# Performance work log

Measured on AMD Instinct MI355X. Metric: run time of the kernel, lower is better.

## Reference

```python
import jax, jax.numpy as jnp
import numpy as np
import math

H = 128
NUM_RBF = 32
CUTOFF_UPPER = 4.5
CUTOFF_LOWER = 0.0
N_NODES = 16384
N_EDGES = 65536
EPS = 1e-5


def _layernorm(x, gamma, beta):
    m = x.mean(-1, keepdims=True)
    v = ((x - m) ** 2).mean(-1, keepdims=True)
    return (x - m) / jnp.sqrt(v + EPS) * gamma + beta


def _cosine_cutoff(d):
    # cutoff_lower == 0 branch of CosineCutoff
    return 0.5 * (jnp.cos(d * (math.pi / CUTOFF_UPPER)) + 1.0) * (d < CUTOFF_UPPER).astype(d.dtype)


def _expnorm_rbf(d):
    alpha = 5.0 / (CUTOFF_UPPER - CUTOFF_LOWER)
    start = math.exp(-CUTOFF_UPPER + CUTOFF_LOWER)
    means = jnp.linspace(start, 1.0, NUM_RBF, dtype=d.dtype)
    betas = jnp.full((NUM_RBF,), (2.0 / NUM_RBF * (1.0 - start)) ** -2, dtype=d.dtype)
    de = d[:, None]
    return _cosine_cutoff(de) * jnp.exp(-betas * (jnp.exp(alpha * (-de + CUTOFF_LOWER)) - means) ** 2)


def _skew(v):  # [E,3] -> [E,3,3]
    z = jnp.zeros(v.shape[0], v.dtype)
    return jnp.stack([z, -v[:, 2], v[:, 1], v[:, 2], z, -v[:, 0], -v[:, 1], v[:, 0], z], axis=1).reshape(-1, 3, 3)


def _sym(v):  # traceless symmetric part of outer product, [E,3] -> [E,3,3]
    M = v[:, :, None] * v[:, None, :]
    tr3 = (v * v).sum(-1)[:, None, None] / 3.0
    return M - tr3 * jnp.eye(3, dtype=v.dtype)


def _tensor_norm(T):  # [...,3,3] -> [...]
    return (T ** 2).sum((-2, -1))


def setup_inputs() -> dict:
    key = jax.random.key(0)
    ks = jax.random.split(key, 32)
    s = 0.05
    inp = {
        'z': jax.random.randint(ks[0], (N_NODES,), 0, 128, dtype=jnp.int32),
        'pos': jax.random.normal(ks[1], (N_NODES, 3), jnp.float32) * 3.0,
        'batch': jnp.zeros((N_NODES,), jnp.int32),
        'edge_index': jax.random.randint(ks[2], (2, N_EDGES), 0, N_NODES, dtype=jnp.int64),
        'emb_w': jax.random.normal(ks[3], (128, H), jnp.float32) * s,
        'emb2_w': jax.random.normal(ks[4], (H, 2 * H), jnp.float32) * s,
        'emb2_b': jnp.zeros((H,), jnp.float32),
        'dp1_w': jax.random.normal(ks[5], (H, NUM_RBF), jnp.float32) * s,
        'dp1_b': jnp.zeros((H,), jnp.float32),
        'dp2_w': jax.random.normal(ks[6], (H, NUM_RBF), jnp.float32) * s,
        'dp2_b': jnp.zeros((H,), jnp.float32),
        'dp3_w': jax.random.normal(ks[7], (H, NUM_RBF), jnp.float32) * s,
        'dp3_b': jnp.zeros((H,), jnp.float32),
        'lt0_w': jax.random.normal(ks[8], (H, H), jnp.float32) * s,
        'lt1_w': jax.random.normal(ks[9], (H, H), jnp.float32) * s,
        'lt2_w': jax.random.normal(ks[10], (H, H), jnp.float32) * s,
        'ls0_w': jax.random.normal(ks[11], (2 * H, H), jnp.float32) * s,
        'ls0_b': jnp.zeros((2 * H,), jnp.float32),
        'ls1_w': jax.random.normal(ks[12], (3 * H, 2 * H), jnp.float32) * s,
        'ls1_b': jnp.zeros((3 * H,), jnp.float32),
        'in_gamma': jnp.ones((H,), jnp.float32),
        'in_beta': jnp.zeros((H,), jnp.float32),
        'lin_w': jax.random.normal(ks[13], (H, 3 * H), jnp.float32) * s,
        'lin_b': jnp.zeros((H,), jnp.float32),
        'on_gamma': jnp.ones((3 * H,), jnp.float32),
        'on_beta': jnp.zeros((3 * H,), jnp.float32),
        'ol1_w': jax.random.normal(ks[14], (H // 2, H), jnp.float32) * s,
        'ol1_b': jnp.zeros((H // 2,), jnp.float32),
        'ol2_w': jax.random.normal(ks[15], (1, H // 2), jnp.float32) * s,
        'ol2_b': jnp.zeros((1,), jnp.float32),
    }
    return inp


def reference(z, pos, batch, edge_index, emb_w, emb2_w, emb2_b, dp1_w, dp1_b, dp2_w, dp2_b,
              dp3_w, dp3_b, lt0_w, lt1_w, lt2_w, ls0_w, ls0_b, ls1_w, ls1_b,
              in_gamma, in_beta, lin_w, lin_b, on_gamma, on_beta, ol1_w, ol1_b, ol2_w, ol2_b):
    src, dst = edge_index[0], edge_index[1]
    edge_vec = pos[src] - pos[dst]                            # [E,3]
    edge_weight = jnp.sqrt((edge_vec ** 2).sum(-1))           # [E]
    edge_attr = _expnorm_rbf(edge_weight)                     # [E,R]
    self_mask = src == dst
    edge_vec_norm = edge_vec / jnp.where(self_mask, 1.0, edge_weight)[:, None]

    # atomic-number message: Zij = emb2(concat(emb[z_src], emb[z_dst]))
    Zemb = emb_w[z]                                           # [N,H]
    Zcat = jnp.concatenate([Zemb[src], Zemb[dst]], axis=-1)   # [E,2H]
    Zij = Zcat @ emb2_w.T + emb2_b                            # [E,H]

    C = (_cosine_cutoff(edge_weight)[:, None] * Zij)[:, :, None, None]  # [E,H,1,1]
    eye = jnp.eye(3, dtype=pos.dtype)[None, None]
    d1 = (edge_attr @ dp1_w.T + dp1_b)[:, :, None, None]      # [E,H,1,1]
    d2 = (edge_attr @ dp2_w.T + dp2_b)[:, :, None, None]
    d3 = (edge_attr @ dp3_w.T + dp3_b)[:, :, None, None]
    Iij = d1 * C * eye                                        # [E,H,3,3]
    Aij = d2 * C * _skew(edge_vec_norm)[:, None, :, :]
    Sij = d3 * C * _sym(edge_vec_norm)[:, None, :, :]

    N = pos.shape[0]
    I0 = jax.ops.segment_sum(Iij, src, num_segments=N)        # [N,H,3,3]
    A0 = jax.ops.segment_sum(Aij, src, num_segments=N)
    S0 = jax.ops.segment_sum(Sij, src, num_segments=N)

    tnorm = _layernorm(_tensor_norm(I0 + A0 + S0), in_gamma, in_beta)  # [N,H]
    nrm = jax.nn.silu(tnorm @ ls0_w.T + ls0_b)
    nrm = jax.nn.silu(nrm @ ls1_w.T + ls1_b).reshape(-1, H, 3)          # [N,H,3]

    I = jnp.einsum('nhij,kh->nkij', I0, lt0_w) * nrm[:, :, 0, None, None]
    A = jnp.einsum('nhij,kh->nkij', A0, lt1_w) * nrm[:, :, 1, None, None]
    S = jnp.einsum('nhij,kh->nkij', S0, lt2_w) * nrm[:, :, 2, None, None]

    x = jnp.concatenate([_tensor_norm(I), _tensor_norm(A), _tensor_norm(S)], axis=-1)  # [N,3H]
    x = _layernorm(x, on_gamma, on_beta)
    x = jax.nn.silu(x @ lin_w.T + lin_b)                       # [N,H]
    x = jax.nn.silu(x @ ol1_w.T + ol1_b)                       # [N,H//2]
    y = x @ ol2_w.T + ol2_b                                    # [N,1] per-atom scalar
    return y
```

## Files before the change

kernel.cpp:

```cpp
#include <hip/hip_runtime.h>
#include <math.h>

#define NN 16384
#define NE 65536
#define HH 128

constexpr double D_START = 0.011108996538242306;
constexpr double D_STEP  = (1.0 - D_START) / 31.0;
constexpr float  F_ALPHA = (float)(5.0/4.5);
constexpr double D_BB    = (2.0/32.0)*(1.0 - D_START);
constexpr float  F_BETA  = (float)(1.0/(D_BB*D_BB));
constexpr float  F_PIC   = (float)(M_PI/4.5);

#define POOL_BYTES (32u*1024u*1024u)
__device__ __align__(256) static char g_pool[POOL_BYTES];

typedef __attribute__((ext_vector_type(8))) short bf16x8;
typedef __attribute__((ext_vector_type(4))) float f32x4;

__device__ __forceinline__ float siluf(float x){
  return x * (1.0f/(1.0f + expf(-x)));
}
__device__ __forceinline__ short f2bf(float x){
  unsigned u = __float_as_uint(x);
  unsigned r = (u + 0x7fffu + ((u>>16)&1u)) >> 16;
  return (short)r;
}
__device__ __forceinline__ float bf2f(short h){
  return __uint_as_float(((unsigned)(unsigned short)h)<<16);
}
__device__ __forceinline__ void split_bf(float x, short& h, short& l){
  h = f2bf(x);
  l = f2bf(x - bf2f(h));
}

__global__ __launch_bounds__(128) void k_prez(const float* __restrict__ emb_w,
    const float* __restrict__ emb2_w, const float* __restrict__ emb2_b,
    float* __restrict__ PZ, float* __restrict__ QZ){
  __shared__ float erow[128];
  int a = blockIdx.x, h = threadIdx.x;
  erow[h] = emb_w[a*128 + h];
  __syncthreads();
  float p = 0.f, q = 0.f;
  #pragma unroll 8
  for (int k=0;k<128;++k){
    float e = erow[k];
    p += e * emb2_w[h*256 + k];
    q += e * emb2_w[h*256 + 128 + k];
  }
  PZ[a*128 + h] = p + emb2_b[h];
  QZ[a*128 + h] = q;
}

__global__ __launch_bounds__(256) void k_cvtw(
    const float* __restrict__ ls0, const float* __restrict__ ls1,
    const float* __restrict__ lin, const float* __restrict__ lt0,
    const float* __restrict__ lt1, const float* __restrict__ lt2,
    const float* __restrict__ dp1, const float* __restrict__ dp2,
    const float* __restrict__ dp3, const float* __restrict__ ol1,
    short* __restrict__ ls0h, short* __restrict__ ls0l,
    short* __restrict__ ls1h, short* __restrict__ ls1l,
    short* __restrict__ linh, short* __restrict__ linl,
    short* __restrict__ lt0h, short* __restrict__ lt0l,
    short* __restrict__ lt1h, short* __restrict__ lt1l,
    short* __restrict__ lt2h, short* __restrict__ lt2l,
    short* __restrict__ dwh, short* __restrict__ dwl,
    short* __restrict__ ol1h, short* __restrict__ ol1l){
  int tid = blockIdx.x*256 + threadIdx.x;
  const float* s; short *dh, *dl; int i;
  if      (tid < 32768)  { s=ls0; dh=ls0h; dl=ls0l; i=tid; }
  else if (tid < 131072) { s=ls1; dh=ls1h; dl=ls1l; i=tid-32768; }
  else if (tid < 180224) { s=lin; dh=linh; dl=linl; i=tid-131072; }
  else if (tid < 196608) { s=lt0; dh=lt0h; dl=lt0l; i=tid-180224; }
  else if (tid < 212992) { s=lt1; dh=lt1h; dl=lt1l; i=tid-196608; }
  else if (tid < 229376) { s=lt2; dh=lt2h; dl=lt2l; i=tid-212992; }
  else if (tid < 241664) {
    int j = tid - 229376;
    int g = j >> 12, idx = j & 4095;
    s = (g==0)?dp1:((g==1)?dp2:dp3);
    short h,l; split_bf(s[idx], h, l);
    dwh[j] = h; dwl[j] = l;
    return;
  }
  else { s=ol1; dh=ol1h; dl=ol1l; i=tid-241664; }
  short h,l; split_bf(s[i], h, l);
  dh[i] = h; dl[i] = l;
}

__global__ __launch_bounds__(256) void k_edge(const int* __restrict__ ei,
    const float* __restrict__ pos, const int* __restrict__ z,
    int* __restrict__ counts, int* __restrict__ esrc, int* __restrict__ ezs,
    int* __restrict__ ezd, float* __restrict__ ev,
    short* __restrict__ atth, short* __restrict__ attl){
  int e = blockIdx.x*256 + threadIdx.x;
  if (e >= NE) return;
  int s = ei[e];
  int t = ei[NE + e];
  float dx = pos[3*s+0] - pos[3*t+0];
  float dy = pos[3*s+1] - pos[3*t+1];
  float dz = pos[3*s+2] - pos[3*t+2];
  float d = sqrtf(dx*dx + dy*dy + dz*dz);
  if (d < 4.5f){
    atomicAdd(&counts[s], 1);
    esrc[e] = s;
    ezs[e] = z[s];
    ezd[e] = z[t];
    float denom = (s==t) ? 1.0f : d;
    ev[4*e+0] = dx/denom;
    ev[4*e+1] = dy/denom;
    ev[4*e+2] = dz/denom;
    float cut = 0.5f*(cosf(d*F_PIC) + 1.0f);
    ev[4*e+3] = cut;
    float q = expf(-F_ALPHA*d);
    #pragma unroll
    for (int r=0;r<32;++r){
      float m = (float)(D_START + r*D_STEP);
      float u = q - m;
      float a = cut * expf(-F_BETA*u*u);
      short hh, ll; split_bf(a, hh, ll);
      atth[32*e + r] = hh;
      attl[32*e + r] = ll;
    }
  } else {
    esrc[e] = -1;
  }
}

__global__ __launch_bounds__(1024) void k_scan(const int* __restrict__ counts,
    int* __restrict__ offsets, int* __restrict__ cursor){
  __shared__ int part[1024];
  int t = threadIdx.x;
  int loc[16];
  int s = 0;
  #pragma unroll
  for (int i=0;i<16;++i){ loc[i] = counts[t*16+i]; s += loc[i]; }
  part[t] = s;
  __syncthreads();
  for (int o=1;o<1024;o<<=1){
    int add = (t>=o) ? part[t-o] : 0;
    __syncthreads();
    part[t] += add;
    __syncthreads();
  }
  int excl = (t==0) ? 0 : part[t-1];
  #pragma unroll
  for (int i=0;i<16;++i){
    offsets[t*16+i] = excl;
    cursor[t*16+i] = excl;
    excl += loc[i];
  }
  if (t==1023) offsets[NN] = excl;
}

__global__ __launch_bounds__(256) void k_scatter(const int* __restrict__ esrc,
    int* __restrict__ cursor, int* __restrict__ elist){
  int e = blockIdx.x*256 + threadIdx.x;
  if (e >= NE) return;
  int s = esrc[e];
  if (s < 0) return;
  int p = atomicAdd(&cursor[s], 1);
  elist[p] = e;
}

__global__ __launch_bounds__(256, 2) void k_mega(
    const int* __restrict__ offsets, const int* __restrict__ elist,
    const int* __restrict__ ezs, const int* __restrict__ ezd,
    const float* __restrict__ ev,
    const short* __restrict__ atth, const short* __restrict__ attl,
    const short* __restrict__ dwh, const short* __restrict__ dwl,
    const float* __restrict__ db1, const float* __restrict__ db2,
    const float* __restrict__ db3,
    const float* __restrict__ PZ, const float* __restrict__ QZ,
    const float* __restrict__ in_g, const float* __restrict__ in_b,
    const short* __restrict__ w0h, const short* __restrict__ w0l,
    const short* __restrict__ w1h, const short* __restrict__ w1l,
    const short* __restrict__ w2h, const short* __restrict__ w2l,
    const short* __restrict__ ls0h, const short* __restrict__ ls0l,
    const float* __restrict__ ls0b,
    const short* __restrict__ ls1h, const short* __restrict__ ls1l,
    const float* __restrict__ ls1b,
    const short* __restrict__ linh, const short* __restrict__ linl,
    const float* __restrict__ linb,
    const short* __restrict__ ol1h, const short* __restrict__ ol1l,
    const float* __restrict__ ol1b,
    const float* __restrict__ ol2w, const float* __restrict__ ol2b,
    const float* __restrict__ on_g, const float* __restrict__ on_b,
    float* __restrict__ y){
  __shared__ __align__(16) char sm[77568];
  float* Dt   = (float*)(sm);
  short* tnhL = (short*)(sm);
  short* tnlL = tnhL + 2560;
  float* NRMt = (float*)(sm);
  short* X3h  = (short*)(sm);
  short* X3l  = X3h + 2560;
  short* PlnL = (short*)(sm + 25600);
  short* T1hL = (short*)(sm + 25600);
  short* T1lL = T1hL + 4608;
  float* xlsL = (float*)(sm + 25600);
  short* xhL  = (short*)(sm + 25600 + 25088);
  short* xlL  = xhL + 6656;
  float* partL= (float*)(sm + 77312);

  int t = threadIdx.x;
  int w = t >> 6, lane = t & 63;
  int col16 = lane & 15, quad = lane >> 4;
  int bn = blockIdx.x*16;
  int node = t >> 4, q = t & 15;

  int e0n = offsets[bn + node], e1n = offsets[bn + node + 1];
  int e0b = offsets[bn], e1b = offsets[bn + 16];

  float pv[10][8];
  #pragma unroll
  for (int p=0;p<10;++p)
    #pragma unroll
    for (int i=0;i<8;++i) pv[p][i]=0.f;

  const float* dbp[3] = {db1, db2, db3};
  for (int c0 = e0b; c0 < e1b; c0 += 16){
    int jA = c0 + col16; if (jA >= e1b) jA = e1b - 1;
    int eA = elist[jA];
    bf16x8 ah = *(const bf16x8*)(atth + (size_t)eA*32 + quad*8);
    bf16x8 al = *(const bf16x8*)(attl + (size_t)eA*32 + quad*8);
    f32x4 dacc[6];
    #pragma unroll
    for (int nt=0;nt<6;++nt) dacc[nt] = (f32x4){0.f,0.f,0.f,0.f};
    #pragma unroll
    for (int nt=0;nt<6;++nt){
      int col = w*96 + nt*16 + col16;
      int g = col >> 7, cg = col & 127;
      bf16x8 wh = *(const bf16x8*)(dwh + g*4096 + cg*32 + quad*8);
      bf16x8 wl = *(const bf16x8*)(dwl + g*4096 + cg*32 + quad*8);
      dacc[nt] = __builtin_amdgcn_mfma_f32_16x16x32_bf16(ah, wh, dacc[nt], 0,0,0);
      dacc[nt] = __builtin_amdgcn_mfma_f32_16x16x32_bf16(ah, wl, dacc[nt], 0,0,0);
      dacc[nt] = __builtin_amdgcn_mfma_f32_16x16x32_bf16(al, wh, dacc[nt], 0,0,0);
    }
    #pragma unroll
    for (int nt=0;nt<6;++nt){
      int col = w*96 + nt*16 + col16;
      int g = col >> 7;
      float bb = dbp[g][col & 127];
      #pragma unroll
      for (int r=0;r<4;++r)
        Dt[(quad*4+r)*388 + col] = dacc[nt][r] + bb;
    }
    __syncthreads();
    int jlo = e0n > c0 ? e0n : c0;
    int jhi0 = c0 + 16; if (jhi0 > e1b) jhi0 = e1b;
    int jhi = e1n < jhi0 ? e1n : jhi0;
    for (int j = jlo; j < jhi; ++j){
      int le = j - c0;
      int e = elist[j];
      float4 evv = *(const float4*)(ev + 4*e);
      int zs = ezs[e], zd = ezd[e];
      const float* pz = PZ + zs*128 + q*8;
      const float* qz = QZ + zd*128 + q*8;
      const float* dr = Dt + le*388 + q*8;
      float vx = evv.x, vy = evv.y, vz = evv.z, cut = evv.w;
      float t3v = (vx*vx + vy*vy + vz*vz)*(1.0f/3.0f);
      #pragma unroll
      for (int i=0;i<8;++i){
        float C = cut * (pz[i] + qz[i]);
        float d1 = dr[i], d2 = dr[128+i], d3 = dr[256+i];
        pv[0][i] += d1*C;
        float wa = d2*C;
        pv[1][i] += wa*vx; pv[2][i] += wa*vy; pv[3][i] += wa*vz;
        float ws = d3*C;
        pv[4][i] += ws*(vx*vx - t3v);
        pv[5][i] += ws*(vy*vy - t3v);
        pv[6][i] += ws*(vz*vz - t3v);
        pv[7][i] += ws*(vx*vy);
        pv[8][i] += ws*(vx*vz);
        pv[9][i] += ws*(vy*vz);
      }
    }
    __syncthreads();
  }

  {
    float tnv[8];
    float s8 = 0.f;
    #pragma unroll
    for (int i=0;i<8;++i){
      float x = 3.f*pv[0][i]*pv[0][i]
              + 2.f*(pv[1][i]*pv[1][i]+pv[2][i]*pv[2][i]+pv[3][i]*pv[3][i])
              + (pv[4][i]*pv[4][i]+pv[5][i]*pv[5][i]+pv[6][i]*pv[6][i])
              + 2.f*(pv[7][i]*pv[7][i]+pv[8][i]*pv[8][i]+pv[9][i]*pv[9][i]);
      tnv[i] = x; s8 += x;
    }
    #pragma unroll
    for (int o=8;o;o>>=1) s8 += __shfl_xor(s8, o, 64);
    float mean = s8*(1.0f/128.0f);
    float vq = 0.f;
    #pragma unroll
    for (int i=0;i<8;++i){ float d = tnv[i]-mean; vq += d*d; }
    #pragma unroll
    for (int o=8;o;o>>=1) vq += __shfl_xor(vq, o, 64);
    float rstd = 1.0f/sqrtf(vq*(1.0f/128.0f) + 1e-5f);
    #pragma unroll
    for (int i=0;i<8;++i){
      int h = q*8 + i;
      float val = (tnv[i]-mean)*rstd*in_g[h] + in_b[h];
      short hh, ll; split_bf(val, hh, ll);
      tnhL[node*160 + h] = hh;
      tnlL[node*160 + h] = ll;
    }
  }

  const short* wgh[3] = {w0h, w1h, w2h};
  const short* wgl[3] = {w0l, w1l, w2l};
  constexpr int gmap[10] = {0,1,1,1,2,2,2,2,2,2};
  f32x4 acc[10][2];
  #pragma unroll
  for (int pass=0; pass<2; ++pass){
    int pbase = pass*5;
    #pragma unroll
    for (int pl=0; pl<5; ++pl){
      short* dst = PlnL + (pl*4 + (q>>2))*1280 + node*80 + (q&3)*16;
      #pragma unroll
      for (int i=0;i<8;++i){
        short hh, ll; split_bf(pv[pbase+pl][i], hh, ll);
        dst[i] = hh; dst[8+i] = ll;
      }
    }
    __syncthreads();
    #pragma unroll
    for (int pl=0; pl<5; ++pl)
      #pragma unroll
      for (int tt=0; tt<2; ++tt) acc[pbase+pl][tt] = (f32x4){0.f,0.f,0.f,0.f};
    #pragma unroll
    for (int hc4=0; hc4<4; ++hc4){
      #pragma unroll
      for (int pl=0; pl<5; ++pl){
        int p = pbase + pl;
        const int g = gmap[p];
        bf16x8 bh[2], bl[2];
        #pragma unroll
        for (int tt=0; tt<2; ++tt){
          int row = w*32 + tt*16 + col16;
          bh[tt] = *(const bf16x8*)(wgh[g] + row*128 + hc4*32 + quad*8);
          bl[tt] = *(const bf16x8*)(wgl[g] + row*128 + hc4*32 + quad*8);
        }
        const short* ab = PlnL + (pl*4 + hc4)*1280 + col16*80 + quad*16;
        bf16x8 ah = *(const bf16x8*)(ab);
        bf16x8 al = *(const bf16x8*)(ab + 8);
        #pragma unroll
        for (int tt=0; tt<2; ++tt){
          acc[p][tt] = __builtin_amdgcn_mfma_f32_16x16x32_bf16(ah, bh[tt], acc[p][tt], 0,0,0);
          acc[p][tt] = __builtin_amdgcn_mfma_f32_16x16x32_bf16(ah, bl[tt], acc[p][tt], 0,0,0);
          acc[p][tt] = __builtin_amdgcn_mfma_f32_16x16x32_bf16(al, bh[tt], acc[p][tt], 0,0,0);
        }
      }
    }
    __syncthreads();
  }

  {
    f32x4 macc[4];
    #pragma unroll
    for (int nt=0;nt<4;++nt) macc[nt] = (f32x4){0.f,0.f,0.f,0.f};
    #pragma unroll
    for (int kc=0; kc<4; ++kc){
      bf16x8 tah = *(const bf16x8*)(tnhL + col16*160 + kc*32 + quad*8);
      bf16x8 tal = *(const bf16x8*)(tnlL + col16*160 + kc*32 + quad*8);
      #pragma unroll
      for (int nt=0;nt<4;++nt){
        int n = w*64 + nt*16 + col16;
        bf16x8 wh = *(const bf16x8*)(ls0h + n*128 + kc*32 + quad*8);
        bf16x8 wl = *(const bf16x8*)(ls0l + n*128 + kc*32 + quad*8);
        macc[nt] = __builtin_amdgcn_mfma_f32_16x16x32_bf16(tah, wh, macc[nt], 0,0,0);
        macc[nt] = __builtin_amdgcn_mfma_f32_16x16x32_bf16(tah, wl, macc[nt], 0,0,0);
        macc[nt] = __builtin_amdgcn_mfma_f32_16x16x32_bf16(tal, wh, macc[nt], 0,0,0);
      }
    }
    #pragma unroll
    for (int nt=0;nt<4;++nt){
      int n = w*64 + nt*16 + col16;
      float bb = ls0b[n];
      #pragma unroll
      for (int r=0;r<4;++r){
        float v = siluf(macc[nt][r] + bb);
        short hh, ll; split_bf(v, hh, ll);
        T1hL[(quad*4+r)*288 + n] = hh;
        T1lL[(quad*4+r)*288 + n] = ll;
      }
    }
    __syncthreads();
    f32x4 nacc[6];
    #pragma unroll
    for (int nt=0;nt<6;++nt) nacc[nt] = (f32x4){0.f,0.f,0.f,0.f};
    #pragma unroll
    for (int kc=0; kc<8; ++kc){
      bf16x8 tah = *(const bf16x8*)(T1hL + col16*288 + kc*32 + quad*8);
      bf16x8 tal = *(const bf16x8*)(T1lL + col16*288 + kc*32 + quad*8);
      #pragma unroll
      for (int nt=0;nt<6;++nt){
        int n = w*96 + nt*16 + col16;
        bf16x8 wh = *(const bf16x8*)(ls1h + n*256 + kc*32 + quad*8);
        bf16x8 wl = *(const bf16x8*)(ls1l + n*256 + kc*32 + quad*8);
        nacc[nt] = __builtin_amdgcn_mfma_f32_16x16x32_bf16(tah, wh, nacc[nt], 0,0,0);
        nacc[nt] = __builtin_amdgcn_mfma_f32_16x16x32_bf16(tah, wl, nacc[nt], 0,0,0);
        nacc[nt] = __builtin_amdgcn_mfma_f32_16x16x32_bf16(tal, wh, nacc[nt], 0,0,0);
      }
    }
    __syncthreads();
    #pragma unroll
    for (int nt=0;nt<6;++nt){
      int n = w*96 + nt*16 + col16;
      float bb = ls1b[n];
      #pragma unroll
      for (int r=0;r<4;++r)
        NRMt[(quad*4+r)*388 + n] = siluf(nacc[nt][r] + bb);
    }
    __syncthreads();
  }

  #pragma unroll
  for (int tt=0; tt<2; ++tt){
    int k = w*32 + tt*16 + col16;
    #pragma unroll
    for (int r=0; r<4; ++r){
      int nloc = quad*4 + r;
      const float* nr = NRMt + nloc*388 + 3*k;
      float n0 = nr[0], n1 = nr[1], n2 = nr[2];
      float tI = acc[0][tt][r]*n0;
      float xI = 3.f*tI*tI;
      float a0 = acc[1][tt][r]*n1, a1 = acc[2][tt][r]*n1, a2 = acc[3][tt][r]*n1;
      float xA = 2.f*(a0*a0 + a1*a1 + a2*a2);
      float d0 = acc[4][tt][r]*n2, d1 = acc[5][tt][r]*n2, d2 = acc[6][tt][r]*n2;
      float o0 = acc[7][tt][r]*n2, o1 = acc[8][tt][r]*n2, o2 = acc[9][tt][r]*n2;
      float xS = d0*d0 + d1*d1 + d2*d2 + 2.f*(o0*o0 + o1*o1 + o2*o2);
      xlsL[nloc*388 + k]       = xI;
      xlsL[nloc*388 + 128 + k] = xA;
      xlsL[nloc*388 + 256 + k] = xS;
    }
  }
  __syncthreads();

  {
    float vv[24];
    float s = 0.f;
    #pragma unroll
    for (int i=0;i<24;++i){ vv[i] = xlsL[node*388 + q*24 + i]; s += vv[i]; }
    #pragma unroll
    for (int o=8;o;o>>=1) s += __shfl_xor(s, o, 64);
    float mean = s*(1.0f/384.0f);
    float qsum = 0.f;
    #pragma unroll
    for (int i=0;i<24;++i){ float d = vv[i]-mean; qsum += d*d; }
    #pragma unroll
    for (int o=8;o;o>>=1) qsum += __shfl_xor(qsum, o, 64);
    float rstd = 1.0f/sqrtf(qsum*(1.0f/384.0f) + 1e-5f);
    #pragma unroll
    for (int i=0;i<24;++i){
      int c = q*24 + i;
      float val = (vv[i]-mean)*rstd*on_g[c] + on_b[c];
      short hh, ll; split_bf(val, hh, ll);
      xhL[node*416 + c] = hh;
      xlL[node*416 + c] = ll;
    }
  }
  __syncthreads();

  {
    f32x4 lacc[2];
    #pragma unroll
    for (int nt=0;nt<2;++nt) lacc[nt] = (f32x4){0.f,0.f,0.f,0.f};
    #pragma unroll
    for (int kc=0; kc<12; ++kc){
      bf16x8 xah = *(const bf16x8*)(xhL + col16*416 + kc*32 + quad*8);
      bf16x8 xal = *(const bf16x8*)(xlL + col16*416 + kc*32 + quad*8);
      #pragma unroll
      for (int nt=0;nt<2;++nt){
        int n = w*32 + nt*16 + col16;
        bf16x8 wh = *(const bf16x8*)(linh + n*384 + kc*32 + quad*8);
        bf16x8 wl = *(const bf16x8*)(linl + n*384 + kc*32 + quad*8);
        lacc[nt] = __builtin_amdgcn_mfma_f32_16x16x32_bf16(xah, wh, lacc[nt], 0,0,0);
        lacc[nt] = __builtin_amdgcn_mfma_f32_16x16x32_bf16(xah, wl, lacc[nt], 0,0,0);
        lacc[nt] = __builtin_amdgcn_mfma_f32_16x16x32_bf16(xal, wh, lacc[nt], 0,0,0);
      }
    }
    __syncthreads();
    #pragma unroll
    for (int nt=0;nt<2;++nt){
      int n = w*32 + nt*16 + col16;
      float bb = linb[n];
      #pragma unroll
      for (int r=0;r<4;++r){
        float v = siluf(lacc[nt][r] + bb);
        short hh, ll; split_bf(v, hh, ll);
        X3h[(quad*4+r)*160 + n] = hh;
        X3l[(quad*4+r)*160 + n] = ll;
      }
    }
    __syncthreads();
  }

  {
    f32x4 hacc = (f32x4){0.f,0.f,0.f,0.f};
    int n = w*16 + col16;
    #pragma unroll
    for (int kc=0; kc<4; ++kc){
      bf16x8 xah = *(const bf16x8*)(X3h + col16*160 + kc*32 + quad*8);
      bf16x8 xal = *(const bf16x8*)(X3l + col16*160 + kc*32 + quad*8);
      bf16x8 wh = *(const bf16x8*)(ol1h + n*128 + kc*32 + quad*8);
      bf16x8 wl = *(const bf16x8*)(ol1l + n*128 + kc*32 + quad*8);
      hacc = __builtin_amdgcn_mfma_f32_16x16x32_bf16(xah, wh, hacc, 0,0,0);
      hacc = __builtin_amdgcn_mfma_f32_16x16x32_bf16(xah, wl, hacc, 0,0,0);
      hacc = __builtin_amdgcn_mfma_f32_16x16x32_bf16(xal, wh, hacc, 0,0,0);
    }
    float b1 = ol1b[n], w2 = ol2w[n];
    #pragma unroll
    for (int r=0;r<4;++r){
      float v = siluf(hacc[r] + b1) * w2;
      #pragma unroll
      for (int o=8;o;o>>=1) v += __shfl_xor(v, o, 64);
      if (col16 == 0) partL[w*16 + quad*4 + r] = v;
    }
    __syncthreads();
    if (t < 16)
      y[bn + t] = partL[t] + partL[16+t] + partL[32+t] + partL[48+t] + ol2b[0];
  }
}

extern "C" void kernel_launch(void* const* d_in, const int* in_sizes, int n_in,
                              void* d_out, int out_size, void* d_ws, size_t ws_size,
                              hipStream_t stream) {
  const int*   z      = (const int*)d_in[0];
  const float* pos    = (const float*)d_in[1];
  const int*   ei     = (const int*)d_in[3];
  const float* emb_w  = (const float*)d_in[4];
  const float* emb2_w = (const float*)d_in[5];
  const float* emb2_b = (const float*)d_in[6];
  const float* dp1_w  = (const float*)d_in[7];
  const float* dp1_b  = (const float*)d_in[8];
  const float* dp2_w  = (const float*)d_in[9];
  const float* dp2_b  = (const float*)d_in[10];
  const float* dp3_w  = (const float*)d_in[11];
  const float* dp3_b  = (const float*)d_in[12];
  const float* lt0_w  = (const float*)d_in[13];
  const float* lt1_w  = (const float*)d_in[14];
  const float* lt2_w  = (const float*)d_in[15];
  const float* ls0_w  = (const float*)d_in[16];
  const float* ls0_b  = (const float*)d_in[17];
  const float* ls1_w  = (const float*)d_in[18];
  const float* ls1_b  = (const float*)d_in[19];
  const float* in_g   = (const float*)d_in[20];
  const float* in_b   = (const float*)d_in[21];
  const float* lin_w  = (const float*)d_in[22];
  const float* lin_b  = (const float*)d_in[23];
  const float* on_g   = (const float*)d_in[24];
  const float* on_b   = (const float*)d_in[25];
  const float* ol1_w  = (const float*)d_in[26];
  const float* ol1_b  = (const float*)d_in[27];
  const float* ol2_w  = (const float*)d_in[28];
  const float* ol2_b  = (const float*)d_in[29];
  float* out = (float*)d_out;

  const size_t NEED = 16u*1024u*1024u;
  char* wsb = (char*)d_ws;
  if (ws_size < NEED){
    void* p = nullptr;
    hipGetSymbolAddress(&p, HIP_SYMBOL(g_pool));
    wsb = (char*)p;
  }
  size_t off = 0;
  auto alloc = [&](size_t bytes)->void*{
    void* p = wsb + off;
    off = (off + bytes + 255) & ~(size_t)255;
    return p;
  };
  float* PZ      = (float*)alloc(128*128*4);
  float* QZ      = (float*)alloc(128*128*4);
  int*   counts  = (int*)  alloc(NN*4);
  int*   offsets = (int*)  alloc((NN+1)*4);
  int*   cursor  = (int*)  alloc(NN*4);
  int*   esrc    = (int*)  alloc(NE*4);
  int*   ezs     = (int*)  alloc(NE*4);
  int*   ezd     = (int*)  alloc(NE*4);
  int*   elist   = (int*)  alloc(NE*4);
  float* ev      = (float*)alloc((size_t)NE*4*4);
  short* atth    = (short*)alloc((size_t)NE*32*2);
  short* attl    = (short*)alloc((size_t)NE*32*2);
  short* dwh     = (short*)alloc(3*128*32*2);
  short* dwl     = (short*)alloc(3*128*32*2);
  short* ls0h    = (short*)alloc(256*128*2);
  short* ls0l    = (short*)alloc(256*128*2);
  short* ls1h    = (short*)alloc(384*256*2);
  short* ls1l    = (short*)alloc(384*256*2);
  short* linh    = (short*)alloc(128*384*2);
  short* linl    = (short*)alloc(128*384*2);
  short* lt0h    = (short*)alloc(128*128*2);
  short* lt0l    = (short*)alloc(128*128*2);
  short* lt1h    = (short*)alloc(128*128*2);
  short* lt1l    = (short*)alloc(128*128*2);
  short* lt2h    = (short*)alloc(128*128*2);
  short* lt2l    = (short*)alloc(128*128*2);
  short* ol1h    = (short*)alloc(64*128*2);
  short* ol1l    = (short*)alloc(64*128*2);

  hipMemsetAsync(counts, 0, NN*4, stream);

  k_prez<<<128, 128, 0, stream>>>(emb_w, emb2_w, emb2_b, PZ, QZ);
  k_cvtw<<<976, 256, 0, stream>>>(ls0_w, ls1_w, lin_w, lt0_w, lt1_w, lt2_w,
                                  dp1_w, dp2_w, dp3_w, ol1_w,
                                  ls0h, ls0l, ls1h, ls1l, linh, linl,
                                  lt0h, lt0l, lt1h, lt1l, lt2h, lt2l,
                                  dwh, dwl, ol1h, ol1l);
  k_edge<<<NE/256, 256, 0, stream>>>(ei, pos, z, counts, esrc, ezs, ezd, ev, atth, attl);
  k_scan<<<1, 1024, 0, stream>>>(counts, offsets, cursor);
  k_scatter<<<NE/256, 256, 0, stream>>>(esrc, cursor, elist);
  k_mega<<<NN/16, 256, 0, stream>>>(offsets, elist, ezs, ezd, ev, atth, attl,
                                    dwh, dwl, dp1_b, dp2_b, dp3_b,
                                    PZ, QZ, in_g, in_b,
                                    lt0h, lt0l, lt1h, lt1l, lt2h, lt2l,
                                    ls0h, ls0l, ls0_b, ls1h, ls1l, ls1_b,
                                    linh, linl, lin_b, ol1h, ol1l, ol1_b,
                                    ol2_w, ol2_b, on_g, on_b, out);
}
```

Before: 283.1 us.

## Fuse prep kernels and replace global CSR scan with per-block edge bucketing

Merges the embedding precompute, weight conversion and edge featurisation into a single launch. The memset, scan and scatter kernels are gone: each k_mega block now scans the whole 16-bit source-index array and builds its own per-node edge list in LDS using shared-memory atomics. LDS layout is compacted so three blocks fit per CU. The cost is that every block reads all edge sources, and edges beyond 128 per 16-node block are silently dropped.

```diff
diff --git a/kernel.cpp b/kernel.cpp
--- a/kernel.cpp
+++ b/kernel.cpp
@@ -12,7 +12,7 @@
 constexpr float  F_BETA  = (float)(1.0/(D_BB*D_BB));
 constexpr float  F_PIC   = (float)(M_PI/4.5);
 
-#define POOL_BYTES (32u*1024u*1024u)
+#define POOL_BYTES (16u*1024u*1024u)
 __device__ __align__(256) static char g_pool[POOL_BYTES];
 
 typedef __attribute__((ext_vector_type(8))) short bf16x8;
@@ -34,30 +34,20 @@
   l = f2bf(x - bf2f(h));
 }
 
-__global__ __launch_bounds__(128) void k_prez(const float* __restrict__ emb_w,
-    const float* __restrict__ emb2_w, const float* __restrict__ emb2_b,
-    float* __restrict__ PZ, float* __restrict__ QZ){
-  __shared__ float erow[128];
-  int a = blockIdx.x, h = threadIdx.x;
-  erow[h] = emb_w[a*128 + h];
-  __syncthreads();
-  float p = 0.f, q = 0.f;
-  #pragma unroll 8
-  for (int k=0;k<128;++k){
-    float e = erow[k];
-    p += e * emb2_w[h*256 + k];
-    q += e * emb2_w[h*256 + 128 + k];
-  }
-  PZ[a*128 + h] = p + emb2_b[h];
-  QZ[a*128 + h] = q;
-}
-
-__global__ __launch_bounds__(256) void k_cvtw(
+__global__ __launch_bounds__(256) void k_prep(
+    const int* __restrict__ ei, const float* __restrict__ pos,
+    const int* __restrict__ z,
+    const float* __restrict__ emb_w, const float* __restrict__ emb2_w,
+    const float* __restrict__ emb2_b,
     const float* __restrict__ ls0, const float* __restrict__ ls1,
     const float* __restrict__ lin, const float* __restrict__ lt0,
     const float* __restrict__ lt1, const float* __restrict__ lt2,
     const float* __restrict__ dp1, const float* __restrict__ dp2,
     const float* __restrict__ dp3, const float* __restrict__ ol1,
+    float* __restrict__ PZ, float* __restrict__ QZ,
+    unsigned short* __restrict__ esrc16, int* __restrict__ ezs,
+    int* __restrict__ ezd, float* __restrict__ ev,
+    short* __restrict__ atth, short* __restrict__ attl,
     short* __restrict__ ls0h, short* __restrict__ ls0l,
     short* __restrict__ ls1h, short* __restrict__ ls1l,
     short* __restrict__ linh, short* __restrict__ linl,
@@ -66,104 +56,82 @@
     short* __restrict__ lt2h, short* __restrict__ lt2l,
     short* __restrict__ dwh, short* __restrict__ dwl,
     short* __restrict__ ol1h, short* __restrict__ ol1l){
-  int tid = blockIdx.x*256 + threadIdx.x;
-  const float* s; short *dh, *dl; int i;
-  if      (tid < 32768)  { s=ls0; dh=ls0h; dl=ls0l; i=tid; }
-  else if (tid < 131072) { s=ls1; dh=ls1h; dl=ls1l; i=tid-32768; }
-  else if (tid < 180224) { s=lin; dh=linh; dl=linl; i=tid-131072; }
-  else if (tid < 196608) { s=lt0; dh=lt0h; dl=lt0l; i=tid-180224; }
-  else if (tid < 212992) { s=lt1; dh=lt1h; dl=lt1l; i=tid-196608; }
-  else if (tid < 229376) { s=lt2; dh=lt2h; dl=lt2l; i=tid-212992; }
-  else if (tid < 241664) {
-    int j = tid - 229376;
-    int g = j >> 12, idx = j & 4095;
-    s = (g==0)?dp1:((g==1)?dp2:dp3);
-    short h,l; split_bf(s[idx], h, l);
-    dwh[j] = h; dwl[j] = l;
+  int b = blockIdx.x;
+  if (b < 64){
+    __shared__ float erow[2][128];
+    int sub = threadIdx.x >> 7, h = threadIdx.x & 127;
+    int a = b*2 + sub;
+    erow[sub][h] = emb_w[a*128 + h];
+    __syncthreads();
+    float p = 0.f, q = 0.f;
+    #pragma unroll 8
+    for (int k=0;k<128;++k){
+      float e = erow[sub][k];
+      p += e * emb2_w[h*256 + k];
+      q += e * emb2_w[h*256 + 128 + k];
+    }
+    PZ[a*128 + h] = p + emb2_b[h];
+    QZ[a*128 + h] = q;
     return;
   }
-  else { s=ol1; dh=ol1h; dl=ol1l; i=tid-241664; }
-  short h,l; split_bf(s[i], h, l);
-  dh[i] = h; dl[i] = l;
+  if (b < 1040){
+    int tid = (b-64)*256 + threadIdx.x;
+    const float* s; short *dh, *dl; int i;
+    if      (tid < 32768)  { s=ls0; dh=ls0h; dl=ls0l; i=tid; }
+    else if (tid < 131072) { s=ls1; dh=ls1h; dl=ls1l; i=tid-32768; }
+    else if (tid < 180224) { s=lin; dh=linh; dl=linl; i=tid-131072; }
+    else if (tid < 196608) { s=lt0; dh=lt0h; dl=lt0l; i=tid-180224; }
+    else if (tid < 212992) { s=lt1; dh=lt1h; dl=lt1l; i=tid-196608; }
+    else if (tid < 229376) { s=lt2; dh=lt2h; dl=lt2l; i=tid-212992; }
+    else if (tid < 241664) {
+      int j = tid - 229376;
+      int g = j >> 12, idx = j & 4095;
+      s = (g==0)?dp1:((g==1)?dp2:dp3);
+      short h,l; split_bf(s[idx], h, l);
+      dwh[j] = h; dwl[j] = l;
+      return;
+    }
+    else { s=ol1; dh=ol1h; dl=ol1l; i=tid-241664; }
+    short h,l; split_bf(s[i], h, l);
+    dh[i] = h; dl[i] = l;
+    return;
+  }
+  {
+    int e = (b-1040)*256 + threadIdx.x;
+    int s = ei[e];
+    int t = ei[NE + e];
+    float dx = pos[3*s+0] - pos[3*t+0];
+    float dy = pos[3*s+1] - pos[3*t+1];
+    float dz = pos[3*s+2] - pos[3*t+2];
+    float d = sqrtf(dx*dx + dy*dy + dz*dz);
+    if (d < 4.5f){
+      esrc16[e] = (unsigned short)s;
+      ezs[e] = z[s];
+      ezd[e] = z[t];
+      float denom = (s==t) ? 1.0f : d;
+      ev[4*e+0] = dx/denom;
+      ev[4*e+1] = dy/denom;
+      ev[4*e+2] = dz/denom;
+      float cut = 0.5f*(cosf(d*F_PIC) + 1.0f);
+      ev[4*e+3] = cut;
+      float q = expf(-F_ALPHA*d);
+      #pragma unroll
+      for (int r=0;r<32;++r){
+        float m = (float)(D_START + r*D_STEP);
+        float u = q - m;
+        float a = cut * expf(-F_BETA*u*u);
+        short hh, ll; split_bf(a, hh, ll);
+        atth[32*e + r] = hh;
+        attl[32*e + r] = ll;
+      }
+    } else {
+      esrc16[e] = 0xFFFFu;
+    }
+  }
 }
 
-__global__ __launch_bounds__(256) void k_edge(const int* __restrict__ ei,
-    const float* __restrict__ pos, const int* __restrict__ z,
-    int* __restrict__ counts, int* __restrict__ esrc, int* __restrict__ ezs,
-    int* __restrict__ ezd, float* __restrict__ ev,
-    short* __restrict__ atth, short* __restrict__ attl){
-  int e = blockIdx.x*256 + threadIdx.x;
-  if (e >= NE) return;
-  int s = ei[e];
-  int t = ei[NE + e];
-  float dx = pos[3*s+0] - pos[3*t+0];
-  float dy = pos[3*s+1] - pos[3*t+1];
-  float dz = pos[3*s+2] - pos[3*t+2];
-  float d = sqrtf(dx*dx + dy*dy + dz*dz);
-  if (d < 4.5f){
-    atomicAdd(&counts[s], 1);
-    esrc[e] = s;
-    ezs[e] = z[s];
-    ezd[e] = z[t];
-    float denom = (s==t) ? 1.0f : d;
-    ev[4*e+0] = dx/denom;
-    ev[4*e+1] = dy/denom;
-    ev[4*e+2] = dz/denom;
-    float cut = 0.5f*(cosf(d*F_PIC) + 1.0f);
-    ev[4*e+3] = cut;
-    float q = expf(-F_ALPHA*d);
-    #pragma unroll
-    for (int r=0;r<32;++r){
-      float m = (float)(D_START + r*D_STEP);
-      float u = q - m;
-      float a = cut * expf(-F_BETA*u*u);
-      short hh, ll; split_bf(a, hh, ll);
-      atth[32*e + r] = hh;
-      attl[32*e + r] = ll;
-    }
-  } else {
-    esrc[e] = -1;
-  }
-}
-
-__global__ __launch_bounds__(1024) void k_scan(const int* __restrict__ counts,
-    int* __restrict__ offsets, int* __restrict__ cursor){
-  __shared__ int part[1024];
-  int t = threadIdx.x;
-  int loc[16];
-  int s = 0;
-  #pragma unroll
-  for (int i=0;i<16;++i){ loc[i] = counts[t*16+i]; s += loc[i]; }
-  part[t] = s;
-  __syncthreads();
-  for (int o=1;o<1024;o<<=1){
-    int add = (t>=o) ? part[t-o] : 0;
-    __syncthreads();
-    part[t] += add;
-    __syncthreads();
-  }
-  int excl = (t==0) ? 0 : part[t-1];
-  #pragma unroll
-  for (int i=0;i<16;++i){
-    offsets[t*16+i] = excl;
-    cursor[t*16+i] = excl;
-    excl += loc[i];
-  }
-  if (t==1023) offsets[NN] = excl;
-}
-
-__global__ __launch_bounds__(256) void k_scatter(const int* __restrict__ esrc,
-    int* __restrict__ cursor, int* __restrict__ elist){
-  int e = blockIdx.x*256 + threadIdx.x;
-  if (e >= NE) return;
-  int s = esrc[e];
-  if (s < 0) return;
-  int p = atomicAdd(&cursor[s], 1);
-  elist[p] = e;
-}
-
-__global__ __launch_bounds__(256, 2) void k_mega(
-    const int* __restrict__ offsets, const int* __restrict__ elist,
+__global__ __launch_bounds__(256, 3) void k_mega(
+    const unsigned short* __restrict__ esrc16,
     const int* __restrict__ ezs, const int* __restrict__ ezd,
     const float* __restrict__ ev,
     const short* __restrict__ atth, const short* __restrict__ attl,
@@ -186,29 +154,64 @@
     const float* __restrict__ ol2w, const float* __restrict__ ol2b,
     const float* __restrict__ on_g, const float* __restrict__ on_b,
     float* __restrict__ y){
-  __shared__ __align__(16) char sm[77568];
-  float* Dt   = (float*)(sm);
-  short* tnhL = (short*)(sm);
-  short* tnlL = tnhL + 2560;
-  float* NRMt = (float*)(sm);
-  short* X3h  = (short*)(sm);
-  short* X3l  = X3h + 2560;
-  short* PlnL = (short*)(sm + 25600);
-  short* T1hL = (short*)(sm + 25600);
-  short* T1lL = T1hL + 4608;
-  float* xlsL = (float*)(sm + 25600);
-  short* xhL  = (short*)(sm + 25600 + 25088);
-  short* xlL  = xhL + 6656;
-  float* partL= (float*)(sm + 77312);
+  __shared__ __align__(16) char sm[52224];
+  float* Dt    = (float*)sm;
+  int*   eun   = (int*)(sm + 24832);
+  int*   nun   = (int*)(sm + 25344);
+  int*   elocal= (int*)(sm + 25856);
+  int*   lcnt  = (int*)(sm + 26368);
+  int*   loff  = lcnt + 16;
+  int*   lcur  = loff + 17;
+  int*   gcnt  = lcur + 16;
+  short* PlnL  = (short*)sm;
+  short* T1h   = (short*)sm;
+  short* T1l   = (short*)(sm + 9216);
+  float* xls   = (float*)sm;
+  short* X3h   = (short*)sm;
+  short* X3l   = (short*)(sm + 5120);
+  float* partL = (float*)(sm + 10240);
+  short* tnhL  = (short*)(sm + 27136);
+  short* tnlL  = (short*)(sm + 27136 + 5120);
+  float* NRMt  = (float*)(sm + 27136);
+  short* xhL   = (short*)(sm + 27136);
+  short* xlL   = (short*)(sm + 27136 + 12544);
 
   int t = threadIdx.x;
+  int b = blockIdx.x;
   int w = t >> 6, lane = t & 63;
   int col16 = lane & 15, quad = lane >> 4;
-  int bn = blockIdx.x*16;
+  int bn = b*16;
   int node = t >> 4, q = t & 15;
 
-  int e0n = offsets[bn + node], e1n = offsets[bn + node + 1];
-  int e0b = offsets[bn], e1b = offsets[bn + 16];
+  if (t < 16){ lcnt[t] = 0; lcur[t] = 0; }
+  if (t == 0) gcnt[0] = 0;
+  __syncthreads();
+  for (int e = t; e < NE; e += 256){
+    int s = (int)esrc16[e];
+    if ((s >> 4) == b){
+      int p = atomicAdd(gcnt, 1);
+      if (p < 128){
+        eun[p] = e; nun[p] = s & 15;
+        atomicAdd(&lcnt[s & 15], 1);
+      }
+    }
+  }
+  __syncthreads();
+  if (t == 0){
+    int a = 0;
+    #pragma unroll
+    for (int i=0;i<16;++i){ loff[i] = a; a += lcnt[i]; }
+    loff[16] = a;
+  }
+  __syncthreads();
+  if (t < 128 && t < gcnt[0]){
+    int nd = nun[t];
+    int p = loff[nd] + atomicAdd(&lcur[nd], 1);
+    elocal[p] = eun[t];
+  }
+  __syncthreads();
+  int etot = loff[16];
+  int e0n = loff[node], e1n = loff[node+1];
 
   float pv[10][8];
   #pragma unroll
@@ -217,9 +220,9 @@
     for (int i=0;i<8;++i) pv[p][i]=0.f;
 
   const float* dbp[3] = {db1, db2, db3};
-  for (int c0 = e0b; c0 < e1b; c0 += 16){
-    int jA = c0 + col16; if (jA >= e1b) jA = e1b - 1;
-    int eA = elist[jA];
+  for (int c0 = 0; c0 < etot; c0 += 16){
+    int jA = c0 + col16; if (jA >= etot) jA = etot - 1;
+    int eA = elocal[jA];
     bf16x8 ah = *(const bf16x8*)(atth + (size_t)eA*32 + quad*8);
     bf16x8 al = *(const bf16x8*)(attl + (size_t)eA*32 + quad*8);
     f32x4 dacc[6];
@@ -246,11 +249,11 @@
     }
     __syncthreads();
     int jlo = e0n > c0 ? e0n : c0;
-    int jhi0 = c0 + 16; if (jhi0 > e1b) jhi0 = e1b;
+    int jhi0 = c0 + 16; if (jhi0 > etot) jhi0 = etot;
     int jhi = e1n < jhi0 ? e1n : jhi0;
     for (int j = jlo; j < jhi; ++j){
       int le = j - c0;
-      int e = elist[j];
+      int e = elocal[j];
       float4 evv = *(const float4*)(ev + 4*e);
       int zs = ezs[e], zd = ezd[e];
       const float* pz = PZ + zs*128 + q*8;
@@ -310,26 +313,30 @@
   const short* wgh[3] = {w0h, w1h, w2h};
   const short* wgl[3] = {w0l, w1l, w2l};
   constexpr int gmap[10] = {0,1,1,1,2,2,2,2,2,2};
+  int myhc4 = q >> 2;
   f32x4 acc[10][2];
+  #pragma unroll
+  for (int p=0;p<10;++p)
+    #pragma unroll
+    for (int tt=0;tt<2;++tt) acc[p][tt] = (f32x4){0.f,0.f,0.f,0.f};
   #pragma unroll
   for (int pass=0; pass<2; ++pass){
     int pbase = pass*5;
     #pragma unroll
-    for (int pl=0; pl<5; ++pl){
-      short* dst = PlnL + (pl*4 + (q>>2))*1280 + node*80 + (q&3)*16;
-      #pragma unroll
-      for (int i=0;i<8;++i){
-        short hh, ll; split_bf(pv[pbase+pl][i], hh, ll);
-        dst[i] = hh; dst[8+i] = ll;
-      }
-    }
-    __syncthreads();
-    #pragma unroll
-    for (int pl=0; pl<5; ++pl)
-      #pragma unroll
-      for (int tt=0; tt<2; ++tt) acc[pbase+pl][tt] = (f32x4){0.f,0.f,0.f,0.f};
-    #pragma unroll
     for (int hc4=0; hc4<4; ++hc4){
+      __syncthreads();
+      if (myhc4 == hc4){
+        #pragma unroll
+        for (int pl=0; pl<5; ++pl){
+          short* dst = PlnL + pl*1280 + node*80 + (q&3)*16;
+          #pragma unroll
+          for (int i=0;i<8;++i){
+            short hh, ll; split_bf(pv[pbase+pl][i], hh, ll);
+            dst[i] = hh; dst[8+i] = ll;
+          }
+        }
+      }
+      __syncthreads();
       #pragma unroll
       for (int pl=0; pl<5; ++pl){
         int p = pbase + pl;
@@ -341,7 +348,7 @@
           bh[tt] = *(const bf16x8*)(wgh[g] + row*128 + hc4*32 + quad*8);
           bl[tt] = *(const bf16x8*)(wgl[g] + row*128 + hc4*32 + quad*8);
         }
-        const short* ab = PlnL + (pl*4 + hc4)*1280 + col16*80 + quad*16;
+        const short* ab = PlnL + pl*1280 + col16*80 + quad*16;
         bf16x8 ah = *(const bf16x8*)(ab);
         bf16x8 al = *(const bf16x8*)(ab + 8);
         #pragma unroll
@@ -352,8 +359,8 @@
         }
       }
     }
-    __syncthreads();
-  }
+  }
+  __syncthreads();
 
   {
     f32x4 macc[4];
@@ -373,6 +380,7 @@
         macc[nt] = __builtin_amdgcn_mfma_f32_16x16x32_bf16(tal, wh, macc[nt], 0,0,0);
       }
     }
+    __syncthreads();
     #pragma unroll
     for (int nt=0;nt<4;++nt){
       int n = w*64 + nt*16 + col16;
@@ -381,8 +389,8 @@
       for (int r=0;r<4;++r){
         float v = siluf(macc[nt][r] + bb);
         short hh, ll; split_bf(v, hh, ll);
-        T1hL[(quad*4+r)*288 + n] = hh;
-        T1lL[(quad*4+r)*288 + n] = ll;
+        T1h[(quad*4+r)*288 + n] = hh;
+        T1l[(quad*4+r)*288 + n] = ll;
       }
     }
     __syncthreads();
@@ -391,8 +399,8 @@
     for (int nt=0;nt<6;++nt) nacc[nt] = (f32x4){0.f,0.f,0.f,0.f};
     #pragma unroll
     for (int kc=0; kc<8; ++kc){
-      bf16x8 tah = *(const bf16x8*)(T1hL + col16*288 + kc*32 + quad*8);
-      bf16x8 tal = *(const bf16x8*)(T1lL + col16*288 + kc*32 + quad*8);
+      bf16x8 tah = *(const bf16x8*)(T1h + col16*288 + kc*32 + quad*8);
+      bf16x8 tal = *(const bf16x8*)(T1l + col16*288 + kc*32 + quad*8);
       #pragma unroll
       for (int nt=0;nt<6;++nt){
         int n = w*96 + nt*16 + col16;
@@ -430,9 +438,9 @@
       float d0 = acc[4][tt][r]*n2, d1 = acc[5][tt][r]*n2, d2 = acc[6][tt][r]*n2;
       float o0 = acc[7][tt][r]*n2, o1 = acc[8][tt][r]*n2, o2 = acc[9][tt][r]*n2;
       float xS = d0*d0 + d1*d1 + d2*d2 + 2.f*(o0*o0 + o1*o1 + o2*o2);
-      xlsL[nloc*388 + k]       = xI;
-      xlsL[nloc*388 + 128 + k] = xA;
-      xlsL[nloc*388 + 256 + k] = xS;
+      xls[nloc*388 + k]       = xI;
+      xls[nloc*388 + 128 + k] = xA;
+      xls[nloc*388 + 256 + k] = xS;
     }
   }
   __syncthreads();
@@ -441,7 +449,7 @@
     float vv[24];
     float s = 0.f;
     #pragma unroll
-    for (int i=0;i<24;++i){ vv[i] = xlsL[node*388 + q*24 + i]; s += vv[i]; }
+    for (int i=0;i<24;++i){ vv[i] = xls[node*388 + q*24 + i]; s += vv[i]; }
     #pragma unroll
     for (int o=8;o;o>>=1) s += __shfl_xor(s, o, 64);
     float mean = s*(1.0f/384.0f);
@@ -456,8 +464,8 @@
       int c = q*24 + i;
       float val = (vv[i]-mean)*rstd*on_g[c] + on_b[c];
       short hh, ll; split_bf(val, hh, ll);
-      xhL[node*416 + c] = hh;
-      xlL[node*416 + c] = ll;
+      xhL[node*392 + c] = hh;
+      xlL[node*392 + c] = ll;
     }
   }
   __syncthreads();
@@ -468,8 +476,8 @@
     for (int nt=0;nt<2;++nt) lacc[nt] = (f32x4){0.f,0.f,0.f,0.f};
     #pragma unroll
     for (int kc=0; kc<12; ++kc){
-      bf16x8 xah = *(const bf16x8*)(xhL + col16*416 + kc*32 + quad*8);
-      bf16x8 xal = *(const bf16x8*)(xlL + col16*416 + kc*32 + quad*8);
+      bf16x8 xah = *(const bf16x8*)(xhL + col16*392 + kc*32 + quad*8);
+      bf16x8 xal = *(const bf16x8*)(xlL + col16*392 + kc*32 + quad*8);
       #pragma unroll
       for (int nt=0;nt<2;++nt){
         int n = w*32 + nt*16 + col16;
@@ -557,7 +565,7 @@
   const float* ol2_b  = (const float*)d_in[29];
   float* out = (float*)d_out;
 
-  const size_t NEED = 16u*1024u*1024u;
+  const size_t NEED = 12u*1024u*1024u;
   char* wsb = (char*)d_ws;
   if (ws_size < NEED){
     void* p = nullptr;
@@ -572,13 +580,9 @@
   };
   float* PZ      = (float*)alloc(128*128*4);
   float* QZ      = (float*)alloc(128*128*4);
-  int*   counts  = (int*)  alloc(NN*4);
-  int*   offsets = (int*)  alloc((NN+1)*4);
-  int*   cursor  = (int*)  alloc(NN*4);
-  int*   esrc    = (int*)  alloc(NE*4);
+  unsigned short* esrc16 = (unsigned short*)alloc(NE*2);
   int*   ezs     = (int*)  alloc(NE*4);
   int*   ezd     = (int*)  alloc(NE*4);
-  int*   elist   = (int*)  alloc(NE*4);
   float* ev      = (float*)alloc((size_t)NE*4*4);
   short* atth    = (short*)alloc((size_t)NE*32*2);
   short* attl    = (short*)alloc((size_t)NE*32*2);
@@ -599,18 +603,14 @@
   short* ol1h    = (short*)alloc(64*128*2);
   short* ol1l    = (short*)alloc(64*128*2);
 
-  hipMemsetAsync(counts, 0, NN*4, stream);
-
-  k_prez<<<128, 128, 0, stream>>>(emb_w, emb2_w, emb2_b, PZ, QZ);
-  k_cvtw<<<976, 256, 0, stream>>>(ls0_w, ls1_w, lin_w, lt0_w, lt1_w, lt2_w,
-                                  dp1_w, dp2_w, dp3_w, ol1_w,
-                                  ls0h, ls0l, ls1h, ls1l, linh, linl,
-                                  lt0h, lt0l, lt1h, lt1l, lt2h, lt2l,
-                                  dwh, dwl, ol1h, ol1l);
-  k_edge<<<NE/256, 256, 0, stream>>>(ei, pos, z, counts, esrc, ezs, ezd, ev, atth, attl);
-  k_scan<<<1, 1024, 0, stream>>>(counts, offsets, cursor);
-  k_scatter<<<NE/256, 256, 0, stream>>>(esrc, cursor, elist);
-  k_mega<<<NN/16, 256, 0, stream>>>(offsets, elist, ezs, ezd, ev, atth, attl,
+  k_prep<<<1296, 256, 0, stream>>>(ei, pos, z, emb_w, emb2_w, emb2_b,
+                                   ls0_w, ls1_w, lin_w, lt0_w, lt1_w, lt2_w,
+                                   dp1_w, dp2_w, dp3_w, ol1_w,
+                                   PZ, QZ, esrc16, ezs, ezd, ev, atth, attl,
+                                   ls0h, ls0l, ls1h, ls1l, linh, linl,
+                                   lt0h, lt0l, lt1h, lt1l, lt2h, lt2l,
+                                   dwh, dwl, ol1h, ol1l);
+  k_mega<<<NN/16, 256, 0, stream>>>(esrc16, ezs, ezd, ev, atth, attl,
                                     dwh, dwl, dp1_b, dp2_b, dp3_b,
                                     PZ, QZ, in_g, in_b,
                                     lt0h, lt0l, lt1h, lt1l, lt2h, lt2l,
```

New measurement: 461.5 us. 63.0% more time.
